# Optimization experiments

Hardware: AMD Instinct MI355X
Metric: run time of the kernel (lower is better)

## Reference

```python
import jax, jax.numpy as jnp
import numpy as np

N = 50000
E = 800000
IN_DIM, HID, OUT = 128, 256, 256


def setup_inputs() -> dict:
    key = jax.random.key(0)
    ks = jax.random.split(key, 6)
    x = jax.random.normal(ks[0], (N, IN_DIM), dtype=jnp.float32)
    edge_index = jax.random.randint(ks[1], (2, E), 0, N, dtype=jnp.int64)
    W1 = jax.random.normal(ks[2], (IN_DIM, HID), dtype=jnp.float32) / np.sqrt(IN_DIM)
    b1 = jnp.zeros((HID,), dtype=jnp.float32)
    W2 = jax.random.normal(ks[3], (HID, OUT), dtype=jnp.float32) / np.sqrt(HID)
    b2 = jnp.zeros((OUT,), dtype=jnp.float32)
    return {"x": x, "edge_index": edge_index, "W1": W1, "b1": b1, "W2": W2, "b2": b2}


def _gcn_conv(x, edge_index, W, b):
    """PyG GCNConv: add self-loops, symmetric deg^-1/2 norm, linear, scatter-add, bias."""
    n = x.shape[0]
    loops = jnp.arange(n, dtype=edge_index.dtype)
    src = jnp.concatenate([edge_index[0], loops])  # [E+N]
    dst = jnp.concatenate([edge_index[1], loops])  # [E+N]
    deg = jax.ops.segment_sum(jnp.ones(src.shape[0], dtype=x.dtype), dst, num_segments=n)
    dinv = jnp.where(deg > 0, jax.lax.rsqrt(deg), jnp.zeros_like(deg))
    norm = dinv[src] * dinv[dst]  # [E+N]
    h = x @ W  # [N, out] small GEMM before gather (PyG order)
    msg = h[src] * norm[:, None]  # [E+N, out] -- dominant memory traffic
    out = jax.ops.segment_sum(msg, dst, num_segments=n)
    return out + b


def reference(x, edge_index, W1, b1, W2, b2):
    h = jax.nn.relu(_gcn_conv(x, edge_index, W1, b1))
    # dropout is identity in eval mode
    out = _gcn_conv(h, edge_index, W2, b2)
    # F.normalize(p=2, dim=-1, eps=1e-12)
    nrm = jnp.maximum(jnp.linalg.norm(out, axis=-1, keepdims=True), 1e-12)
    return out / nrm
```

## Files before the change

kernel.cpp:

```cpp
#include <hip/hip_runtime.h>
#include <hip/hip_bf16.h>


#define NNODE 50000
#define FDIM 256
#define SCAN_CHUNK 2048
#define CAST_BLOCKS 3125
#define WCONV_BLOCKS 48

typedef __attribute__((ext_vector_type(8))) short short8;
typedef __attribute__((ext_vector_type(4))) float f32x4;

__device__ __forceinline__ float bflo(unsigned int u) {
    union { unsigned int i; float f; } c;
    c.i = u << 16;
    return c.f;
}
__device__ __forceinline__ float bfhi(unsigned int u) {
    union { unsigned int i; float f; } c;
    c.i = u & 0xFFFF0000u;
    return c.f;
}
__device__ __forceinline__ unsigned short f2bf(float f) {
    __hip_bfloat16 h = __float2bfloat16(f);
    return *reinterpret_cast<unsigned short*>(&h);
}
__device__ __forceinline__ unsigned int pk(float lo, float hi) {
    return (unsigned int)f2bf(lo) | ((unsigned int)f2bf(hi) << 16);
}

__global__ __launch_bounds__(256) void prep_kernel(
    const float* __restrict__ x, unsigned int* __restrict__ xb,
    const float* __restrict__ W1, unsigned short* __restrict__ Wf1,
    const float* __restrict__ W2, unsigned short* __restrict__ Wf2,
    const int* __restrict__ ei, int* __restrict__ counts, int E) {
    int b = blockIdx.x, t = threadIdx.x;
    if (b < CAST_BLOCKS) {
        int i = b * 256 + t;
        const float4* xf = reinterpret_cast<const float4*>(x);
        float4 p = xf[2 * i], q = xf[2 * i + 1];
        uint4 o;
        o.x = pk(p.x, p.y); o.y = pk(p.z, p.w);
        o.z = pk(q.x, q.y); o.w = pk(q.z, q.w);
        reinterpret_cast<uint4*>(xb)[i] = o;
    } else if (b < CAST_BLOCKS + WCONV_BLOCKS) {
        int idx = (b - CAST_BLOCKS) * 256 + t;
        const float* W;
        unsigned short* Wf;
        if (idx < 16 * 256) { W = W1; Wf = Wf1; }
        else { idx -= 16 * 256; W = W2; Wf = Wf2; }
        int g = idx >> 8, c = idx & 255;
        ushort4 lo = make_ushort4(f2bf(W[(8 * g + 0) * 256 + c]), f2bf(W[(8 * g + 1) * 256 + c]),
                                  f2bf(W[(8 * g + 2) * 256 + c]), f2bf(W[(8 * g + 3) * 256 + c]));
        ushort4 hi = make_ushort4(f2bf(W[(8 * g + 4) * 256 + c]), f2bf(W[(8 * g + 5) * 256 + c]),
                                  f2bf(W[(8 * g + 6) * 256 + c]), f2bf(W[(8 * g + 7) * 256 + c]));
        *reinterpret_cast<ushort4*>(&Wf[(size_t)idx * 8]) = lo;
        *reinterpret_cast<ushort4*>(&Wf[(size_t)idx * 8 + 4]) = hi;
    } else {
        int e = (b - CAST_BLOCKS - WCONV_BLOCKS) * 256 + t;
        if (e < E) atomicAdd(&counts[ei[E + e]], 1);
    }
}

__global__ __launch_bounds__(256) void scan_part1(const int* __restrict__ counts,
                                                  int* __restrict__ bsum, int n) {
    __shared__ int ws[4];
    int b = blockIdx.x, t = threadIdx.x;
    int base = b * SCAN_CHUNK + t * 8;
    int s = 0;
#pragma unroll
    for (int j = 0; j < 8; ++j) {
        int i = base + j;
        if (i < n) s += counts[i];
    }
#pragma unroll
    for (int off = 32; off >= 1; off >>= 1) s += __shfl_xor(s, off, 64);
    if ((t & 63) == 0) ws[t >> 6] = s;
    __syncthreads();
    if (t == 0) bsum[b] = ws[0] + ws[1] + ws[2] + ws[3];
}

__global__ void scan_part2(const int* __restrict__ bsum, int* __restrict__ boff,
                           int* __restrict__ row_ptr, int nb, int n) {
    int l = threadIdx.x;
    int v = (l < nb) ? bsum[l] : 0;
    int incl = v;
#pragma unroll
    for (int off = 1; off < 64; off <<= 1) {
        int u = __shfl_up(incl, off, 64);
        if (l >= off) incl += u;
    }
    if (l < nb) boff[l] = incl - v;
    if (l == nb - 1) row_ptr[n] = incl;
}

__global__ __launch_bounds__(256) void scan_part3(const int* __restrict__ counts,
                                                  const int* __restrict__ boff,
                                                  int* __restrict__ row_ptr,
                                                  int* __restrict__ cursor,
                                                  float* __restrict__ dinv, int n) {
    __shared__ int ws[4];
    int b = blockIdx.x, t = threadIdx.x, lane = t & 63, wid = t >> 6;
    int base = b * SCAN_CHUNK + t * 8;
    int v[8];
    int s = 0;
#pragma unroll
    for (int j = 0; j < 8; ++j) {
        int i = base + j;
        v[j] = (i < n) ? counts[i] : 0;
        s += v[j];
    }
    int incl = s;
#pragma unroll
    for (int off = 1; off < 64; off <<= 1) {
        int u = __shfl_up(incl, off, 64);
        if (lane >= off) incl += u;
    }
    if (lane == 63) ws[wid] = incl;
    __syncthreads();
    int woff = 0;
    for (int u = 0; u < wid; ++u) woff += ws[u];
    int ex = boff[b] + woff + incl - s;
#pragma unroll
    for (int j = 0; j < 8; ++j) {
        int i = base + j;
        if (i < n) {
            row_ptr[i] = ex;
            cursor[i] = ex;
            dinv[i] = rsqrtf((float)(v[j] + 1));
        }
        ex += v[j];
    }
}

__global__ void fill_kernel(const int* __restrict__ ei, const float* __restrict__ dinv,
                            int* __restrict__ cursor, int2* __restrict__ edata, int E) {
    int e = blockIdx.x * blockDim.x + threadIdx.x;
    if (e < E) {
        int s = ei[e];
        int d = ei[E + e];
        int pos = atomicAdd(&cursor[d], 1);
        float nm = dinv[s] * dinv[d];
        edata[pos] = make_int2(s, __float_as_int(nm));
    }
}

__global__ __launch_bounds__(256) void agg1_kernel(const unsigned int* __restrict__ xb,
                                                   const int* __restrict__ rowp,
                                                   const int2* __restrict__ edata,
                                                   const float* __restrict__ dinv,
                                                   unsigned int* __restrict__ A1, int n) {
    int node = (blockIdx.x << 2) + (threadIdx.x >> 6);
    if (node >= n) return;
    int lane = threadIdx.x & 63;
    float di = dinv[node];
    float d2 = di * di;
    unsigned int sv = xb[(size_t)node * 64 + lane];
    float a0 = bflo(sv) * d2, a1 = bfhi(sv) * d2;
    int beg = rowp[node], end = rowp[node + 1];
    for (int e = beg; e < end; e += 4) {
        int2 ed[4];
        unsigned int v[4];
#pragma unroll
        for (int k = 0; k < 4; ++k) {
            int ee = e + k;
            ed[k] = (ee < end) ? edata[ee] : make_int2(node, 0);
        }
#pragma unroll
        for (int k = 0; k < 4; ++k) v[k] = xb[(size_t)ed[k].x * 64 + lane];
#pragma unroll
        for (int k = 0; k < 4; ++k) {
            float nm = __int_as_float(ed[k].y);
            a0 = fmaf(bflo(v[k]), nm, a0);
            a1 = fmaf(bfhi(v[k]), nm, a1);
        }
    }
    A1[(size_t)node * 64 + lane] = pk(a0, a1);
}

__global__ __launch_bounds__(256) void agg2_kernel(const uint2* __restrict__ hb,
                                                   const int* __restrict__ rowp,
                                                   const int2* __restrict__ edata,
                                                   const float* __restrict__ dinv,
                                                   uint2* __restrict__ A2, int n) {
    int node = (blockIdx.x << 2) + (threadIdx.x >> 6);
    if (node >= n) return;
    int lane = threadIdx.x & 63;
    float di = dinv[node];
    float d2 = di * di;
    uint2 sv = hb[(size_t)node * 64 + lane];
    float a0 = bflo(sv.x) * d2, a1 = bfhi(sv.x) * d2;
    float a2 = bflo(sv.y) * d2, a3 = bfhi(sv.y) * d2;
    int beg = rowp[node], end = rowp[node + 1];
    for (int e = beg; e < end; e += 4) {
        int2 ed[4];
        uint2 v[4];
#pragma unroll
        for (int k = 0; k < 4; ++k) {
            int ee = e + k;
            ed[k] = (ee < end) ? edata[ee] : make_int2(node, 0);
        }
#pragma unroll
        for (int k = 0; k < 4; ++k) v[k] = hb[(size_t)ed[k].x * 64 + lane];
#pragma unroll
        for (int k = 0; k < 4; ++k) {
            float nm = __int_as_float(ed[k].y);
            a0 = fmaf(bflo(v[k].x), nm, a0);
            a1 = fmaf(bfhi(v[k].x), nm, a1);
            a2 = fmaf(bflo(v[k].y), nm, a2);
            a3 = fmaf(bfhi(v[k].y), nm, a3);
        }
    }
    uint2 o;
    o.x = pk(a0, a1);
    o.y = pk(a2, a3);
    A2[(size_t)node * 64 + lane] = o;
}

template <int K, int EPI>
__global__ __launch_bounds__(256) void gemm_fused(const unsigned short* __restrict__ A,
                                                  const unsigned short* __restrict__ Wf,
                                                  const float* __restrict__ bias,
                                                  void* __restrict__ outp, int n) {
    __shared__ unsigned short As[64 * K];
    __shared__ __align__(16) float ssred[64][4];
    int t = threadIdx.x;
    int row0 = blockIdx.x * 64;

#pragma unroll
    for (int i = 0; i < (64 * K) / (8 * 256); ++i) {
        int o = 8 * (t + 256 * i);
        int row = o / K, k = o % K;
        int srow = row0 + row;
        uint4 v = make_uint4(0u, 0u, 0u, 0u);
        if (srow < n) v = *reinterpret_cast<const uint4*>(&A[(size_t)srow * K + k]);
        int gx = (k >> 3) ^ (row & 7);
        *reinterpret_cast<uint4*>(&As[row * K + gx * 8]) = v;
    }
    __syncthreads();

    int lane = t & 63, wv = t >> 6;
    int l15 = lane & 15, lhi = lane >> 4;
    f32x4 zero = {0.f, 0.f, 0.f, 0.f};
    f32x4 acc[4][4];
#pragma unroll
    for (int rf = 0; rf < 4; ++rf)
#pragma unroll
        for (int cf = 0; cf < 4; ++cf) acc[rf][cf] = zero;

#pragma unroll
    for (int s = 0; s < K / 32; ++s) {
        int g = 4 * s + lhi;
        short8 a[4], b[4];
#pragma unroll
        for (int rf = 0; rf < 4; ++rf) {
            int row = 16 * rf + l15;
            a[rf] = *reinterpret_cast<const short8*>(&As[row * K + (g ^ (row & 7)) * 8]);
        }
#pragma unroll
        for (int cf = 0; cf < 4; ++cf) {
            int c = 64 * wv + 16 * cf + l15;
            b[cf] = *reinterpret_cast<const short8*>(&Wf[((size_t)g * 256 + c) * 8]);
        }
#pragma unroll
        for (int rf = 0; rf < 4; ++rf)
#pragma unroll
            for (int cf = 0; cf < 4; ++cf)
                acc[rf][cf] = __builtin_amdgcn_mfma_f32_16x16x32_bf16(a[rf], b[cf], acc[rf][cf], 0, 0, 0);
    }

    if constexpr (EPI == 0) {
        unsigned short* H = (unsigned short*)outp;
#pragma unroll
        for (int cf = 0; cf < 4; ++cf) {
            int col = 64 * wv + 16 * cf + l15;
            float bc = bias[col];
#pragma unroll
            for (int rf = 0; rf < 4; ++rf) {
#pragma unroll
                for (int j = 0; j < 4; ++j) {
                    int row = row0 + 16 * rf + 4 * lhi + j;
                    if (row < n) H[(size_t)row * 256 + col] = f2bf(fmaxf(acc[rf][cf][j] + bc, 0.f));
                }
            }
        }
    } else {
        float* O = (float*)outp;
        float ss[4][4];
#pragma unroll
        for (int rf = 0; rf < 4; ++rf)
#pragma unroll
            for (int j = 0; j < 4; ++j) ss[rf][j] = 0.f;
#pragma unroll
        for (int cf = 0; cf < 4; ++cf) {
            int col = 64 * wv + 16 * cf + l15;
            float bc = bias[col];
#pragma unroll
            for (int rf = 0; rf < 4; ++rf)
#pragma unroll
                for (int j = 0; j < 4; ++j) {
                    float v = acc[rf][cf][j] + bc;
                    acc[rf][cf][j] = v;
                    ss[rf][j] = fmaf(v, v, ss[rf][j]);
                }
        }
#pragma unroll
        for (int rf = 0; rf < 4; ++rf)
#pragma unroll
            for (int j = 0; j < 4; ++j) {
#pragma unroll
                for (int off = 1; off <= 8; off <<= 1)
                    ss[rf][j] += __shfl_xor(ss[rf][j], off, 64);
            }
        if (l15 == 0) {
#pragma unroll
            for (int rf = 0; rf < 4; ++rf)
#pragma unroll
                for (int j = 0; j < 4; ++j) ssred[16 * rf + 4 * lhi + j][wv] = ss[rf][j];
        }
        __syncthreads();
        float rinv[4][4];
#pragma unroll
        for (int rf = 0; rf < 4; ++rf)
#pragma unroll
            for (int j = 0; j < 4; ++j) {
                float4 s4 = *reinterpret_cast<const float4*>(ssred[16 * rf + 4 * lhi + j]);
                float tot = s4.x + s4.y + s4.z + s4.w;
                rinv[rf][j] = 1.f / fmaxf(sqrtf(tot), 1e-12f);
            }
#pragma unroll
        for (int cf = 0; cf < 4; ++cf) {
            int col = 64 * wv + 16 * cf + l15;
#pragma unroll
            for (int rf = 0; rf < 4; ++rf)
#pragma unroll
                for (int j = 0; j < 4; ++j) {
                    int row = row0 + 16 * rf + 4 * lhi + j;
                    if (row < n) O[(size_t)row * 256 + col] = acc[rf][cf][j] * rinv[rf][j];
                }
        }
    }
}

extern "C" void kernel_launch(void* const* d_in, const int* in_sizes, int n_in,
                              void* d_out, int out_size, void* d_ws, size_t ws_size,
                              hipStream_t stream) {
    const float* x  = (const float*)d_in[0];
    const int*   ei = (const int*)d_in[1];
    const float* W1 = (const float*)d_in[2];
    const float* b1 = (const float*)d_in[3];
    const float* W2 = (const float*)d_in[4];
    const float* b2 = (const float*)d_in[5];
    float* out = (float*)d_out;

    const int N = NNODE;
    const int E = in_sizes[1] / 2;
    const int NB = (N + SCAN_CHUNK - 1) / SCAN_CHUNK;

    char* ws = (char*)d_ws;
    size_t off = 0;
    auto alloc = [&](size_t bytes) -> void* {
        void* p = ws + off;
        off = (off + bytes + 255) & ~(size_t)255;
        return p;
    };
    unsigned int*   xb  = (unsigned int*)alloc((size_t)N * 128 * 2);
    unsigned int*   A1  = (unsigned int*)alloc((size_t)N * 128 * 2);
    unsigned short* Bbf = (unsigned short*)alloc((size_t)N * FDIM * 2);
    uint2*          A2  = (uint2*)alloc((size_t)N * FDIM * 2);
    unsigned short* Wf1 = (unsigned short*)alloc((size_t)16 * 256 * 8 * 2);
    unsigned short* Wf2 = (unsigned short*)alloc((size_t)32 * 256 * 8 * 2);
    int*   counts = (int*)alloc((size_t)N * 4);
    int*   rowp   = (int*)alloc((size_t)(N + 1) * 4);
    int*   cursor = (int*)alloc((size_t)N * 4);
    float* dinv   = (float*)alloc((size_t)N * 4);
    int2*  edata  = (int2*)alloc((size_t)E * 8);
    int*   bsum   = (int*)alloc((size_t)NB * 4);
    int*   boff   = (int*)alloc((size_t)NB * 4);

    hipMemsetAsync(counts, 0, (size_t)N * 4, stream);
    int count_blocks = (E + 255) / 256;
    prep_kernel<<<CAST_BLOCKS + WCONV_BLOCKS + count_blocks, 256, 0, stream>>>(
        x, xb, W1, Wf1, W2, Wf2, ei, counts, E);
    scan_part1<<<NB, 256, 0, stream>>>(counts, bsum, N);
    scan_part2<<<1, 64, 0, stream>>>(bsum, boff, rowp, NB, N);
    scan_part3<<<NB, 256, 0, stream>>>(counts, boff, rowp, cursor, dinv, N);
    fill_kernel<<<(E + 255) / 256, 256, 0, stream>>>(ei, dinv, cursor, edata, E);

    agg1_kernel<<<(N + 3) / 4, 256, 0, stream>>>(xb, rowp, edata, dinv, A1, N);
    gemm_fused<128, 0><<<(N + 63) / 64, 256, 0, stream>>>(
        (const unsigned short*)A1, Wf1, b1, Bbf, N);
    agg2_kernel<<<(N + 3) / 4, 256, 0, stream>>>(
        (const uint2*)Bbf, rowp, edata, dinv, A2, N);
    gemm_fused<256, 1><<<(N + 63) / 64, 256, 0, stream>>>(
        (const unsigned short*)A2, Wf2, b2, out, N);
}
```

Before: 281.0 us.

## Split each node's edge list across two wavefronts and store bare column indices

The aggregation kernels now give each destination node two wavefronts that take alternate edges, combining the partial sums through shared memory. This adds parallelism for nodes with average degree around 16. The CSR edge array no longer carries a precomputed norm: it stores only source indices, and the norm is rebuilt at aggregation time from dinv[s]*dinv[d]. This halves the edge-record size and removes a dinv lookup from the fill kernel, at the cost of an extra random dinv gather per edge, a block-wide sync, and a simpler unroll without the padded 4-edge batching.

After: 297.4 us. 1.06x slower.

```diff
diff --git a/kernel.cpp b/kernel.cpp
--- a/kernel.cpp
+++ b/kernel.cpp
@@ -133,88 +133,97 @@
     }
 }
 
-__global__ void fill_kernel(const int* __restrict__ ei, const float* __restrict__ dinv,
-                            int* __restrict__ cursor, int2* __restrict__ edata, int E) {
+__global__ void fill_kernel(const int* __restrict__ ei, int* __restrict__ cursor,
+                            int* __restrict__ col, int E) {
     int e = blockIdx.x * blockDim.x + threadIdx.x;
     if (e < E) {
         int s = ei[e];
         int d = ei[E + e];
-        int pos = atomicAdd(&cursor[d], 1);
-        float nm = dinv[s] * dinv[d];
-        edata[pos] = make_int2(s, __float_as_int(nm));
-    }
-}
-
-__global__ __launch_bounds__(256) void agg1_kernel(const unsigned int* __restrict__ xb,
+        col[atomicAdd(&cursor[d], 1)] = s;
+    }
+}
+
+__global__ __launch_bounds__(512) void agg1_kernel(const unsigned int* __restrict__ xb,
                                                    const int* __restrict__ rowp,
-                                                   const int2* __restrict__ edata,
+                                                   const int* __restrict__ col,
                                                    const float* __restrict__ dinv,
                                                    unsigned int* __restrict__ A1, int n) {
-    int node = (blockIdx.x << 2) + (threadIdx.x >> 6);
-    if (node >= n) return;
+    __shared__ float2 part[4][64];
+    int wv = threadIdx.x >> 6;
+    int pair = wv >> 1, sub = wv & 1;
+    int node = (blockIdx.x << 2) + pair;
     int lane = threadIdx.x & 63;
-    float di = dinv[node];
-    float d2 = di * di;
-    unsigned int sv = xb[(size_t)node * 64 + lane];
-    float a0 = bflo(sv) * d2, a1 = bfhi(sv) * d2;
-    int beg = rowp[node], end = rowp[node + 1];
-    for (int e = beg; e < end; e += 4) {
-        int2 ed[4];
-        unsigned int v[4];
-#pragma unroll
-        for (int k = 0; k < 4; ++k) {
-            int ee = e + k;
-            ed[k] = (ee < end) ? edata[ee] : make_int2(node, 0);
-        }
-#pragma unroll
-        for (int k = 0; k < 4; ++k) v[k] = xb[(size_t)ed[k].x * 64 + lane];
-#pragma unroll
-        for (int k = 0; k < 4; ++k) {
-            float nm = __int_as_float(ed[k].y);
-            a0 = fmaf(bflo(v[k]), nm, a0);
-            a1 = fmaf(bfhi(v[k]), nm, a1);
-        }
-    }
-    A1[(size_t)node * 64 + lane] = pk(a0, a1);
-}
-
-__global__ __launch_bounds__(256) void agg2_kernel(const uint2* __restrict__ hb,
+    bool live = node < n;
+    float di = live ? dinv[node] : 0.f;
+    float a0 = 0.f, a1 = 0.f;
+    if (live && !sub) {
+        float d2 = di * di;
+        unsigned int sv = xb[(size_t)node * 64 + lane];
+        a0 = bflo(sv) * d2;
+        a1 = bfhi(sv) * d2;
+    }
+    if (live) {
+        int beg = rowp[node], end = rowp[node + 1];
+#pragma unroll 4
+        for (int e = beg + sub; e < end; e += 2) {
+            int s = col[e];
+            float nm = dinv[s] * di;
+            unsigned int v = xb[(size_t)s * 64 + lane];
+            a0 = fmaf(bflo(v), nm, a0);
+            a1 = fmaf(bfhi(v), nm, a1);
+        }
+    }
+    if (sub) part[pair][lane] = make_float2(a0, a1);
+    __syncthreads();
+    if (live && !sub) {
+        float2 p = part[pair][lane];
+        A1[(size_t)node * 64 + lane] = pk(a0 + p.x, a1 + p.y);
+    }
+}
+
+__global__ __launch_bounds__(512) void agg2_kernel(const uint2* __restrict__ hb,
                                                    const int* __restrict__ rowp,
-                                                   const int2* __restrict__ edata,
+                                                   const int* __restrict__ col,
                                                    const float* __restrict__ dinv,
                                                    uint2* __restrict__ A2, int n) {
-    int node = (blockIdx.x << 2) + (threadIdx.x >> 6);
-    if (node >= n) return;
+    __shared__ float4 part[4][64];
+    int wv = threadIdx.x >> 6;
+    int pair = wv >> 1, sub = wv & 1;
+    int node = (blockIdx.x << 2) + pair;
     int lane = threadIdx.x & 63;
-    float di = dinv[node];
-    float d2 = di * di;
-    uint2 sv = hb[(size_t)node * 64 + lane];
-    float a0 = bflo(sv.x) * d2, a1 = bfhi(sv.x) * d2;
-    float a2 = bflo(sv.y) * d2, a3 = bfhi(sv.y) * d2;
-    int beg = rowp[node], end = rowp[node + 1];
-    for (int e = beg; e < end; e += 4) {
-        int2 ed[4];
-        uint2 v[4];
-#pragma unroll
-        for (int k = 0; k < 4; ++k) {
-            int ee = e + k;
-            ed[k] = (ee < end) ? edata[ee] : make_int2(node, 0);
-        }
-#pragma unroll
-        for (int k = 0; k < 4; ++k) v[k] = hb[(size_t)ed[k].x * 64 + lane];
-#pragma unroll
-        for (int k = 0; k < 4; ++k) {
-            float nm = __int_as_float(ed[k].y);
-            a0 = fmaf(bflo(v[k].x), nm, a0);
-            a1 = fmaf(bfhi(v[k].x), nm, a1);
-            a2 = fmaf(bflo(v[k].y), nm, a2);
-            a3 = fmaf(bfhi(v[k].y), nm, a3);
-        }
-    }
-    uint2 o;
-    o.x = pk(a0, a1);
-    o.y = pk(a2, a3);
-    A2[(size_t)node * 64 + lane] = o;
+    bool live = node < n;
+    float di = live ? dinv[node] : 0.f;
+    float a0 = 0.f, a1 = 0.f, a2 = 0.f, a3 = 0.f;
+    if (live && !sub) {
+        float d2 = di * di;
+        uint2 sv = hb[(size_t)node * 64 + lane];
+        a0 = bflo(sv.x) * d2;
+        a1 = bfhi(sv.x) * d2;
+        a2 = bflo(sv.y) * d2;
+        a3 = bfhi(sv.y) * d2;
+    }
+    if (live) {
+        int beg = rowp[node], end = rowp[node + 1];
+#pragma unroll 4
+        for (int e = beg + sub; e < end; e += 2) {
+            int s = col[e];
+            float nm = dinv[s] * di;
+            uint2 v = hb[(size_t)s * 64 + lane];
+            a0 = fmaf(bflo(v.x), nm, a0);
+            a1 = fmaf(bfhi(v.x), nm, a1);
+            a2 = fmaf(bflo(v.y), nm, a2);
+            a3 = fmaf(bfhi(v.y), nm, a3);
+        }
+    }
+    if (sub) part[pair][lane] = make_float4(a0, a1, a2, a3);
+    __syncthreads();
+    if (live && !sub) {
+        float4 p = part[pair][lane];
+        uint2 o;
+        o.x = pk(a0 + p.x, a1 + p.y);
+        o.y = pk(a2 + p.z, a3 + p.w);
+        A2[(size_t)node * 64 + lane] = o;
+    }
 }
 
 template <int K, int EPI>
@@ -374,7 +383,7 @@
     int*   rowp   = (int*)alloc((size_t)(N + 1) * 4);
     int*   cursor = (int*)alloc((size_t)N * 4);
     float* dinv   = (float*)alloc((size_t)N * 4);
-    int2*  edata  = (int2*)alloc((size_t)E * 8);
+    int*   col    = (int*)alloc((size_t)E * 4);
     int*   bsum   = (int*)alloc((size_t)NB * 4);
     int*   boff   = (int*)alloc((size_t)NB * 4);
 
@@ -385,13 +394,13 @@
     scan_part1<<<NB, 256, 0, stream>>>(counts, bsum, N);
     scan_part2<<<1, 64, 0, stream>>>(bsum, boff, rowp, NB, N);
     scan_part3<<<NB, 256, 0, stream>>>(counts, boff, rowp, cursor, dinv, N);
-    fill_kernel<<<(E + 255) / 256, 256, 0, stream>>>(ei, dinv, cursor, edata, E);
-
-    agg1_kernel<<<(N + 3) / 4, 256, 0, stream>>>(xb, rowp, edata, dinv, A1, N);
+    fill_kernel<<<(E + 255) / 256, 256, 0, stream>>>(ei, cursor, col, E);
+
+    agg1_kernel<<<(N + 3) / 4, 512, 0, stream>>>(xb, rowp, col, dinv, A1, N);
     gemm_fused<128, 0><<<(N + 63) / 64, 256, 0, stream>>>(
         (const unsigned short*)A1, Wf1, b1, Bbf, N);
-    agg2_kernel<<<(N + 3) / 4, 256, 0, stream>>>(
-        (const uint2*)Bbf, rowp, edata, dinv, A2, N);
+    agg2_kernel<<<(N + 3) / 4, 512, 0, stream>>>(
+        (const uint2*)Bbf, rowp, col, dinv, A2, N);
     gemm_fused<256, 1><<<(N + 63) / 64, 256, 0, stream>>>(
         (const unsigned short*)A2, Wf2, b2, out, N);
 }
```
